# Performance work log

Hardware: AMD Instinct MI355X
Metric: run time of the kernel (lower is better)

Reference implementation:

```python
import jax, jax.numpy as jnp
import numpy as np

B, W, F = 16384, 64, 120
EPS = 1e-3  # keras BatchNormalization default epsilon


def _bn(x, g, b, m, v):
    return g * (x - m) * jax.lax.rsqrt(v + EPS) + b


def setup_inputs() -> dict:
    key = jax.random.key(0)
    ks = jax.random.split(key, 32)
    n = lambda i, s: jax.random.normal(ks[i], s, dtype=jnp.float32) * 0.05
    u = lambda i, s: jax.random.uniform(ks[i], s, dtype=jnp.float32) + 0.5
    W3 = W * 3
    return {
        'x': jax.random.normal(ks[0], (B, W, F), dtype=jnp.float32),
        # per-timestep Conv1D: only center tap matters on length-1 seq -> [W, F, 3]
        'conv_w': n(1, (W, F, 3)), 'conv_b': n(2, (W, 3)),
        # eye head
        'e_g1': u(3, (W3,)), 'e_b1': n(4, (W3,)), 'e_m1': n(5, (W3,)), 'e_v1': u(6, (W3,)),
        'e_d1_w': n(7, (W3, W3)), 'e_d1_b': n(8, (W3,)),
        'e_g2': u(9, (W3,)), 'e_b2': n(10, (W3,)), 'e_m2': n(11, (W3,)), 'e_v2': u(12, (W3,)),
        'e_d2_w': n(13, (W3, 2 * F)), 'e_d2_b': n(14, (2 * F,)),
        'e_d3_w': n(15, (2 * F, F)), 'e_d3_b': n(16, (F,)),
        # blink head
        'b_g1': u(17, (W3,)), 'b_b1': n(18, (W3,)), 'b_m1': n(19, (W3,)), 'b_v1': u(20, (W3,)),
        'b_d1_w': n(21, (W3, W)), 'b_d1_b': n(22, (W,)),
        'b_g2': u(23, (W,)), 'b_b2': n(24, (W,)), 'b_m2': n(25, (W,)), 'b_v2': u(26, (W,)),
        'b_d2_w': n(27, (W, W // 2)), 'b_d2_b': n(28, (W // 2,)),
        'b_d3_w': n(29, (W // 2, 1)), 'b_d3_b': n(30, (1,)),
    }


def reference(x, conv_w, conv_b, e_g1, e_b1, e_m1, e_v1, e_d1_w, e_d1_b,
              e_g2, e_b2, e_m2, e_v2, e_d2_w, e_d2_b, e_d3_w, e_d3_b,
              b_g1, b_b1, b_m1, b_v1, b_d1_w, b_d1_b,
              b_g2, b_b2, b_m2, b_v2, b_d2_w, b_d2_b, b_d3_w, b_d3_b):
    # window_size independent Conv1D(k=3,'same') on length-1 sequences reduce to a
    # single batched per-timestep matmul with the center kernel tap.
    combined = jnp.tanh(jnp.einsum('bwf,wfk->bwk', x, conv_w) + conv_b)
    combined = combined.reshape(x.shape[0], -1)  # [B, 3*W]
    # eye-feature head (dropout = identity at inference, BN uses moving stats)
    e = _bn(combined, e_g1, e_b1, e_m1, e_v1)
    e = jnp.tanh(e @ e_d1_w + e_d1_b)
    e = _bn(e, e_g2, e_b2, e_m2, e_v2)
    e = e @ e_d2_w + e_d2_b
    e = e @ e_d3_w + e_d3_b  # [B, F]
    # blink head
    b = _bn(combined, b_g1, b_b1, b_m1, b_v1)
    b = jnp.tanh(b @ b_d1_w + b_d1_b)
    b = _bn(b, b_g2, b_b2, b_m2, b_v2)
    b = jnp.tanh(b @ b_d2_w + b_d2_b)
    b = jax.nn.sigmoid(b @ b_d3_w + b_d3_b)  # [B, 1]
    return jnp.concatenate([e, b], axis=-1)  # [B, F+1]
```

## Files before the change

### kernel.cpp

```cpp
#include <hip/hip_runtime.h>
#include <hip/hip_bf16.h>
#include <string.h>

#define EPSBN 1e-3f

constexpr int kC1  = 192;
constexpr int kN2  = 240;
constexpr int kOut = 121;
constexpr int BTOT = 16384;

typedef __attribute__((ext_vector_type(8))) short bf16x8;
typedef __attribute__((ext_vector_type(4))) float f32x4;

__device__ __forceinline__ unsigned short f2bf(float f) {
  union { float f; unsigned u; } v; v.f = f;
  unsigned r = v.u + 0x7FFFu + ((v.u >> 16) & 1u);
  return (unsigned short)(r >> 16);
}
__device__ __forceinline__ float bf2f(unsigned short h) {
  union { unsigned u; float f; } v; v.u = ((unsigned)h) << 16;
  return v.f;
}

constexpr size_t OFF_W1E  = 0;
constexpr size_t OFF_W2E  = OFF_W1E + 73728;
constexpr size_t OFF_W3E  = OFF_W2E + 92160;
constexpr size_t OFF_W1B  = OFF_W3E + 65536;
constexpr size_t OFF_W2B  = OFF_W1B + 24576;
constexpr size_t OFF_BIAS = OFF_W2B + 4096;
constexpr size_t OFF_CWT  = OFF_BIAS + 2736;
constexpr size_t WS_NEED  = OFF_CWT + 122880;

__global__ __launch_bounds__(256) void prep_cwt(const float* __restrict__ cw,
                                                float* __restrict__ cwt4)
{
  int idx = blockIdx.x * 256 + threadIdx.x;
  if (idx < 7680) {
    int f = idx >> 6, w = idx & 63;
    float4 v;
    v.x = cw[(size_t)w * 360 + f * 3 + 0];
    v.y = cw[(size_t)w * 360 + f * 3 + 1];
    v.z = cw[(size_t)w * 360 + f * 3 + 2];
    v.w = 0.f;
    *reinterpret_cast<float4*>(cwt4 + (size_t)idx * 4) = v;
  }
}

__device__ __forceinline__ void pack_one(unsigned short* dst, int idx,
                                         const float* __restrict__ W, int Ksrc, int Nsrc,
                                         int KS, const float* g, const float* v)
{
  int per_nt = KS * 512;
  int nt = idx / per_nt; int r = idx - nt * per_nt;
  int ks = r >> 9; int r2 = r & 511;
  int l = r2 >> 3; int j = r2 & 7;
  int i = ks * 32 + ((l >> 4) << 3) + j;
  int n = (nt << 4) + (l & 15);
  float val = 0.f;
  if (i < Ksrc && n < Nsrc) {
    float s = g ? g[i] * rsqrtf(v[i] + EPSBN) : 1.f;
    val = s * W[(size_t)i * Nsrc + n];
  }
  dst[idx] = f2bf(val);
}

__global__ __launch_bounds__(256) void prep_pack(
    const float* e_g1, const float* e_v1, const float* e_d1_w,
    const float* e_g2, const float* e_v2, const float* e_d2_w,
    const float* e_d3_w,
    const float* b_g1, const float* b_v1, const float* b_d1_w,
    const float* b_g2, const float* b_v2, const float* b_d2_w,
    unsigned short* W1E, unsigned short* W2E, unsigned short* W3E,
    unsigned short* W1B, unsigned short* W2B)
{
  int e = blockIdx.x * 256 + threadIdx.x;
  if (e < 36864)                       pack_one(W1E, e,          e_d1_w, 192, 192, 6, e_g1, e_v1);
  else if (e < 36864 + 46080)          pack_one(W2E, e - 36864,  e_d2_w, 192, 240, 6, e_g2, e_v2);
  else if (e < 82944 + 32768)          pack_one(W3E, e - 82944,  e_d3_w, 240, 120, 8, nullptr, nullptr);
  else if (e < 115712 + 12288)         pack_one(W1B, e - 115712, b_d1_w, 192, 64,  6, b_g1, b_v1);
  else if (e < 128000 + 2048)          pack_one(W2B, e - 128000, b_d2_w, 64,  32,  2, b_g2, b_v2);
}

__global__ __launch_bounds__(256) void prep_bias(
    const float* e_g1, const float* e_b1, const float* e_m1, const float* e_v1,
    const float* e_d1_w, const float* e_d1_b,
    const float* e_g2, const float* e_b2, const float* e_m2, const float* e_v2,
    const float* e_d2_w, const float* e_d2_b, const float* e_d3_b,
    const float* b_g1, const float* b_b1, const float* b_m1, const float* b_v1,
    const float* b_d1_w, const float* b_d1_b,
    const float* b_g2, const float* b_b2, const float* b_m2, const float* b_v2,
    const float* b_d2_w, const float* b_d2_b,
    const float* b_d3_w, const float* b_d3_b,
    float* BIAS)
{
  int q = blockIdx.x * 256 + threadIdx.x;
  if (q < 192) {
    int j = q; float acc = e_d1_b[j];
    for (int i = 0; i < 192; ++i) {
      float s = e_g1[i] * rsqrtf(e_v1[i] + EPSBN);
      acc += (e_b1[i] - e_m1[i] * s) * e_d1_w[(size_t)i * 192 + j];
    }
    BIAS[q] = acc;
  } else if (q < 432) {
    int j = q - 192; float acc = e_d2_b[j];
    for (int i = 0; i < 192; ++i) {
      float s = e_g2[i] * rsqrtf(e_v2[i] + EPSBN);
      acc += (e_b2[i] - e_m2[i] * s) * e_d2_w[(size_t)i * 240 + j];
    }
    BIAS[q] = acc;
  } else if (q < 552) {
    BIAS[q] = e_d3_b[q - 432];
  } else if (q < 616) {
    int j = q - 552; float acc = b_d1_b[j];
    for (int i = 0; i < 192; ++i) {
      float s = b_g1[i] * rsqrtf(b_v1[i] + EPSBN);
      acc += (b_b1[i] - b_m1[i] * s) * b_d1_w[(size_t)i * 64 + j];
    }
    BIAS[q] = acc;
  } else if (q < 648) {
    int j = q - 616; float acc = b_d2_b[j];
    for (int i = 0; i < 64; ++i) {
      float s = b_g2[i] * rsqrtf(b_v2[i] + EPSBN);
      acc += (b_b2[i] - b_m2[i] * s) * b_d2_w[(size_t)i * 32 + j];
    }
    BIAS[q] = acc;
  } else if (q < 680) {
    BIAS[q] = b_d3_w[q - 648];
  } else if (q == 680) {
    BIAS[q] = b_d3_b[0];
  }
}

__global__ __launch_bounds__(64) void fused_all(
    const float* __restrict__ x,
    const float* __restrict__ cwt4, const float* __restrict__ conv_b,
    const unsigned short* __restrict__ W1E, const unsigned short* __restrict__ W2E,
    const unsigned short* __restrict__ W3E, const unsigned short* __restrict__ W1B,
    const unsigned short* __restrict__ W2B, const float* __restrict__ BIAS,
    float* __restrict__ out)
{
  __shared__ __align__(16) short Ac[16 * 200];
  __shared__ __align__(16) char  ubuf[15 * 65 * 16];

  float4* xt = reinterpret_cast<float4*>(ubuf);
  short*  Hs = reinterpret_cast<short*>(ubuf);
  short*  H2 = reinterpret_cast<short*>(ubuf + 6400);

  const int l = threadIdx.x;
  const int R = blockIdx.x * 16;

  {
    const float bc0 = conv_b[l * 3 + 0];
    const float bc1 = conv_b[l * 3 + 1];
    const float bc2 = conv_b[l * 3 + 2];

    for (int r = 0; r < 16; ++r) {
      const float* xrow = x + (size_t)(R + r) * 7680;
      float a0 = 0.f, a1 = 0.f, a2 = 0.f;

      for (int h = 0; h < 2; ++h) {
        #pragma unroll
        for (int i = 0; i < 15; ++i) {
          int g = i * 64 + l;
          int w = g / 15, fs = g - 15 * w;
          float4 v = *reinterpret_cast<const float4*>(xrow + w * 120 + h * 60 + 4 * fs);
          xt[fs * 65 + w] = v;
        }
        __syncthreads();

        #pragma unroll 5
        for (int fq = 0; fq < 15; ++fq) {
          float4 x4 = xt[fq * 65 + l];
          float xs[4] = {x4.x, x4.y, x4.z, x4.w};
          #pragma unroll
          for (int j = 0; j < 4; ++j) {
            int f = h * 60 + 4 * fq + j;
            float4 c4 = *reinterpret_cast<const float4*>(cwt4 + (size_t)(f * 64 + l) * 4);
            a0 = fmaf(xs[j], c4.x, a0);
            a1 = fmaf(xs[j], c4.y, a1);
            a2 = fmaf(xs[j], c4.z, a2);
          }
        }
        __syncthreads();
      }

      Ac[r * 200 + 3 * l + 0] = (short)f2bf(tanhf(a0 + bc0));
      Ac[r * 200 + 3 * l + 1] = (short)f2bf(tanhf(a1 + bc1));
      Ac[r * 200 + 3 * l + 2] = (short)f2bf(tanhf(a2 + bc2));
    }
  }
  __syncthreads();

  #pragma unroll
  for (int e = l; e < 256; e += 64) {
    int row = e >> 4, c = e & 15;
    H2[row * 264 + 240 + c] = 0;
  }

  const int arow = l & 15;
  const int kofs = (l >> 4) * 8;
  const int mb   = (l >> 4) * 4;

  for (int nt = 0; nt < 12; ++nt) {
    f32x4 acc = {0.f, 0.f, 0.f, 0.f};
    const bf16x8* bp = (const bf16x8*)W1E + (size_t)(nt * 6) * 64 + l;
    #pragma unroll
    for (int ks = 0; ks < 6; ++ks) {
      bf16x8 a = *(const bf16x8*)(Ac + arow * 200 + ks * 32 + kofs);
      acc = __builtin_amdgcn_mfma_f32_16x16x32_bf16(a, bp[(size_t)ks * 64], acc, 0, 0, 0);
    }
    int n = nt * 16 + arow;
    float bv = BIAS[n];
    __syncthreads();
    #pragma unroll
    for (int r = 0; r < 4; ++r)
      Hs[(mb + r) * 200 + n] = (short)f2bf(tanhf(acc[r] + bv));
  }
  __syncthreads();

  for (int nt = 0; nt < 15; ++nt) {
    f32x4 acc = {0.f, 0.f, 0.f, 0.f};
    const bf16x8* bp = (const bf16x8*)W2E + (size_t)(nt * 6) * 64 + l;
    #pragma unroll
    for (int ks = 0; ks < 6; ++ks) {
      bf16x8 a = *(const bf16x8*)(Hs + arow * 200 + ks * 32 + kofs);
      acc = __builtin_amdgcn_mfma_f32_16x16x32_bf16(a, bp[(size_t)ks * 64], acc, 0, 0, 0);
    }
    int n = nt * 16 + arow;
    float bv = BIAS[192 + n];
    #pragma unroll
    for (int r = 0; r < 4; ++r)
      H2[(mb + r) * 264 + n] = (short)f2bf(acc[r] + bv);
  }
  __syncthreads();

  for (int nt = 0; nt < 8; ++nt) {
    f32x4 acc = {0.f, 0.f, 0.f, 0.f};
    const bf16x8* bp = (const bf16x8*)W3E + (size_t)(nt * 8) * 64 + l;
    #pragma unroll
    for (int ks = 0; ks < 8; ++ks) {
      bf16x8 a = *(const bf16x8*)(H2 + arow * 264 + ks * 32 + kofs);
      acc = __builtin_amdgcn_mfma_f32_16x16x32_bf16(a, bp[(size_t)ks * 64], acc, 0, 0, 0);
    }
    int n = nt * 16 + arow;
    if (n < 120) {
      float bv = BIAS[432 + n];
      #pragma unroll
      for (int r = 0; r < 4; ++r)
        out[(size_t)(R + mb + r) * kOut + n] = acc[r] + bv;
    }
  }
  __syncthreads();

  for (int nt = 0; nt < 4; ++nt) {
    f32x4 acc = {0.f, 0.f, 0.f, 0.f};
    const bf16x8* bp = (const bf16x8*)W1B + (size_t)(nt * 6) * 64 + l;
    #pragma unroll
    for (int ks = 0; ks < 6; ++ks) {
      bf16x8 a = *(const bf16x8*)(Ac + arow * 200 + ks * 32 + kofs);
      acc = __builtin_amdgcn_mfma_f32_16x16x32_bf16(a, bp[(size_t)ks * 64], acc, 0, 0, 0);
    }
    int n = nt * 16 + arow;
    float bv = BIAS[552 + n];
    #pragma unroll
    for (int r = 0; r < 4; ++r)
      Hs[(mb + r) * 200 + n] = (short)f2bf(tanhf(acc[r] + bv));
  }
  __syncthreads();

  for (int nt = 0; nt < 2; ++nt) {
    f32x4 acc = {0.f, 0.f, 0.f, 0.f};
    const bf16x8* bp = (const bf16x8*)W2B + (size_t)(nt * 2) * 64 + l;
    #pragma unroll
    for (int ks = 0; ks < 2; ++ks) {
      bf16x8 a = *(const bf16x8*)(Hs + arow * 200 + ks * 32 + kofs);
      acc = __builtin_amdgcn_mfma_f32_16x16x32_bf16(a, bp[(size_t)ks * 64], acc, 0, 0, 0);
    }
    int n = nt * 16 + arow;
    float bv = BIAS[616 + n];
    #pragma unroll
    for (int r = 0; r < 4; ++r)
      H2[(mb + r) * 264 + n] = (short)f2bf(tanhf(acc[r] + bv));
  }
  __syncthreads();

  if (l < 16) {
    float s = BIAS[680];
    #pragma unroll
    for (int i = 0; i < 32; ++i)
      s = fmaf(bf2f((unsigned short)H2[l * 264 + i]), BIAS[648 + i], s);
    out[(size_t)(R + l) * kOut + 120] = 1.f / (1.f + expf(-s));
  }
}

constexpr int CSTR = 193;
__global__ __launch_bounds__(64, 4) void fused_blink_fb(
    const float* __restrict__ x,
    const float* __restrict__ conv_w, const float* __restrict__ conv_b,
    const float* __restrict__ e_g1, const float* __restrict__ e_b1,
    const float* __restrict__ e_m1, const float* __restrict__ e_v1,
    const float* __restrict__ e_d1_w, const float* __restrict__ e_d1_b,
    const float* __restrict__ e_g2, const float* __restrict__ e_b2,
    const float* __restrict__ e_m2, const float* __restrict__ e_v2,
    const float* __restrict__ e_d2_w, const float* __restrict__ e_d2_b,
    const float* __restrict__ e_d3_w, const float* __restrict__ e_d3_b,
    const float* __restrict__ b_g1, const float* __restrict__ b_b1,
    const float* __restrict__ b_m1, const float* __restrict__ b_v1,
    const float* __restrict__ b_d1_w, const float* __restrict__ b_d1_b,
    const float* __restrict__ b_g2, const float* __restrict__ b_b2,
    const float* __restrict__ b_m2, const float* __restrict__ b_v2,
    const float* __restrict__ b_d2_w, const float* __restrict__ b_d2_b,
    const float* __restrict__ b_d3_w, const float* __restrict__ b_d3_b,
    float* __restrict__ out)
{
  __shared__ float comb[4 * CSTR];
  __shared__ __align__(16) float Ab[4 * kN2];
  __shared__ __align__(16) float Bb[4 * kN2];
  const int lane = threadIdx.x;
  const int b0   = blockIdx.x * 4;
  {
    const int rcv = lane >> 4, wloc = lane & 15;
    for (int wc = 0; wc < 4; ++wc) {
      const int w = wc * 16 + wloc;
      const float* xr  = x + ((size_t)(b0 + rcv) * 64 + w) * 120;
      const float* cwp = conv_w + (size_t)w * 360;
      float a0 = 0.f, a1 = 0.f, a2 = 0.f;
      for (int t = 0; t < 30; ++t) {
        float4 xv = *reinterpret_cast<const float4*>(xr + 4 * t);
        float4 c0 = *reinterpret_cast<const float4*>(cwp + 12 * t);
        float4 c1 = *reinterpret_cast<const float4*>(cwp + 12 * t + 4);
        float4 c2 = *reinterpret_cast<const float4*>(cwp + 12 * t + 8);
        a0 += xv.x * c0.x + xv.y * c0.w + xv.z * c1.z + xv.w * c2.y;
        a1 += xv.x * c0.y + xv.y * c1.x + xv.z * c1.w + xv.w * c2.z;
        a2 += xv.x * c0.z + xv.y * c1.y + xv.z * c2.x + xv.w * c2.w;
      }
      comb[rcv * CSTR + 3 * w + 0] = tanhf(a0 + conv_b[3 * w + 0]);
      comb[rcv * CSTR + 3 * w + 1] = tanhf(a1 + conv_b[3 * w + 1]);
      comb[rcv * CSTR + 3 * w + 2] = tanhf(a2 + conv_b[3 * w + 2]);
    }
  }
  __syncthreads();
  #define AR(rr) (Ab + (size_t)(rr) * kN2)
  #define BR(rr) (Bb + (size_t)(rr) * kN2)
  #pragma unroll
  for (int q = 0; q < 12; ++q) {
    int rr = q / 3, cc = q % 3;
    int i = cc * 64 + lane;
    float s = e_g1[i] * rsqrtf(e_v1[i] + EPSBN);
    AR(rr)[i] = comb[rr * CSTR + i] * s + (e_b1[i] - e_m1[i] * s);
  }
  __syncthreads();
  {
    float acc[4][3];
    #pragma unroll
    for (int rr = 0; rr < 4; ++rr) { acc[rr][0]=acc[rr][1]=acc[rr][2]=0.f; }
    for (int i = 0; i < kC1; i += 4) {
      float4 v[4];
      #pragma unroll
      for (int rr = 0; rr < 4; ++rr) v[rr] = *reinterpret_cast<const float4*>(AR(rr) + i);
      #pragma unroll
      for (int io = 0; io < 4; ++io) {
        const float* wp = e_d1_w + (size_t)(i + io) * kC1 + lane;
        float w0 = wp[0], w1 = wp[64], w2 = wp[128];
        #pragma unroll
        for (int rr = 0; rr < 4; ++rr) {
          float xv = reinterpret_cast<const float*>(&v[rr])[io];
          acc[rr][0] = fmaf(xv, w0, acc[rr][0]);
          acc[rr][1] = fmaf(xv, w1, acc[rr][1]);
          acc[rr][2] = fmaf(xv, w2, acc[rr][2]);
        }
      }
    }
    #pragma unroll
    for (int c = 0; c < 3; ++c) {
      int j = c * 64 + lane;
      float s  = e_g2[j] * rsqrtf(e_v2[j] + EPSBN);
      float t  = e_b2[j] - e_m2[j] * s;
      float bs = e_d1_b[j];
      #pragma unroll
      for (int rr = 0; rr < 4; ++rr)
        BR(rr)[j] = tanhf(acc[rr][c] + bs) * s + t;
    }
  }
  __syncthreads();
  {
    const bool m3 = (lane < 48);
    float acc[4][4];
    #pragma unroll
    for (int rr = 0; rr < 4; ++rr) { acc[rr][0]=acc[rr][1]=acc[rr][2]=acc[rr][3]=0.f; }
    for (int i = 0; i < kC1; i += 4) {
      float4 v[4];
      #pragma unroll
      for (int rr = 0; rr < 4; ++rr) v[rr] = *reinterpret_cast<const float4*>(BR(rr) + i);
      #pragma unroll
      for (int io = 0; io < 4; ++io) {
        const float* wp = e_d2_w + (size_t)(i + io) * kN2 + lane;
        float w0 = wp[0], w1 = wp[64], w2 = wp[128];
        float w3 = m3 ? wp[192] : 0.f;
        #pragma unroll
        for (int rr = 0; rr < 4; ++rr) {
          float xv = reinterpret_cast<const float*>(&v[rr])[io];
          acc[rr][0] = fmaf(xv, w0, acc[rr][0]);
          acc[rr][1] = fmaf(xv, w1, acc[rr][1]);
          acc[rr][2] = fmaf(xv, w2, acc[rr][2]);
          acc[rr][3] = fmaf(xv, w3, acc[rr][3]);
        }
      }
    }
    #pragma unroll
    for (int c = 0; c < 4; ++c) {
      int j = c * 64 + lane;
      if (c < 3 || m3) {
        float bs = e_d2_b[j];
        #pragma unroll
        for (int rr = 0; rr < 4; ++rr)
          AR(rr)[j] = acc[rr][c] + bs;
      }
    }
  }
  __syncthreads();
  #pragma unroll
  for (int q = 0; q < 12; ++q) {
    int rr = q / 3, cc = q % 3;
    int i = cc * 64 + lane;
    float s = b_g1[i] * rsqrtf(b_v1[i] + EPSBN);
    BR(rr)[i] = comb[rr * CSTR + i] * s + (b_b1[i] - b_m1[i] * s);
  }
  {
    const bool m56 = (lane < 56);
    float acc[4][2];
    #pragma unroll
    for (int rr = 0; rr < 4; ++rr) { acc[rr][0]=acc[rr][1]=0.f; }
    for (int i = 0; i < kN2; i += 4) {
      float4 v[4];
      #pragma unroll
      for (int rr = 0; rr < 4; ++rr) v[rr] = *reinterpret_cast<const float4*>(AR(rr) + i);
      #pragma unroll
      for (int io = 0; io < 4; ++io) {
        const float* wp = e_d3_w + (size_t)(i + io) * 120 + lane;
        float w0 = wp[0];
        float w1 = m56 ? wp[64] : 0.f;
        #pragma unroll
        for (int rr = 0; rr < 4; ++rr) {
          float xv = reinterpret_cast<const float*>(&v[rr])[io];
          acc[rr][0] = fmaf(xv, w0, acc[rr][0]);
          acc[rr][1] = fmaf(xv, w1, acc[rr][1]);
        }
      }
    }
    #pragma unroll
    for (int c = 0; c < 2; ++c) {
      int j = c * 64 + lane;
      if (j < 120) {
        float bs = e_d3_b[j];
        #pragma unroll
        for (int rr = 0; rr < 4; ++rr)
          out[(size_t)(b0 + rr) * kOut + j] = acc[rr][c] + bs;
      }
    }
  }
  __syncthreads();
  {
    float acc[4] = {0.f, 0.f, 0.f, 0.f};
    for (int i = 0; i < kC1; i += 4) {
      float4 v[4];
      #pragma unroll
      for (int rr = 0; rr < 4; ++rr) v[rr] = *reinterpret_cast<const float4*>(BR(rr) + i);
      #pragma unroll
      for (int io = 0; io < 4; ++io) {
        float w0 = b_d1_w[(size_t)(i + io) * 64 + lane];
        #pragma unroll
        for (int rr = 0; rr < 4; ++rr) {
          float xv = reinterpret_cast<const float*>(&v[rr])[io];
          acc[rr] = fmaf(xv, w0, acc[rr]);
        }
      }
    }
    float s  = b_g2[lane] * rsqrtf(b_v2[lane] + EPSBN);
    float t  = b_b2[lane] - b_m2[lane] * s;
    float bs = b_d1_b[lane];
    #pragma unroll
    for (int rr = 0; rr < 4; ++rr)
      AR(rr)[lane] = tanhf(acc[rr] + bs) * s + t;
  }
  __syncthreads();
  {
    const bool m32 = (lane < 32);
    float acc[4] = {0.f, 0.f, 0.f, 0.f};
    for (int i = 0; i < 64; i += 4) {
      float4 v[4];
      #pragma unroll
      for (int rr = 0; rr < 4; ++rr) v[rr] = *reinterpret_cast<const float4*>(AR(rr) + i);
      #pragma unroll
      for (int io = 0; io < 4; ++io) {
        float w0 = m32 ? b_d2_w[(size_t)(i + io) * 32 + lane] : 0.f;
        #pragma unroll
        for (int rr = 0; rr < 4; ++rr) {
          float xv = reinterpret_cast<const float*>(&v[rr])[io];
          acc[rr] = fmaf(xv, w0, acc[rr]);
        }
      }
    }
    if (m32) {
      float bs = b_d2_b[lane];
      #pragma unroll
      for (int rr = 0; rr < 4; ++rr)
        BR(rr)[lane] = tanhf(acc[rr] + bs);
    }
  }
  __syncthreads();
  if (lane < 4) {
    int rr = lane;
    float acc = b_d3_b[0];
    #pragma unroll
    for (int i = 0; i < 32; ++i)
      acc = fmaf(BR(rr)[i], b_d3_w[i], acc);
    out[(size_t)(b0 + rr) * kOut + 120] = 1.f / (1.f + expf(-acc));
  }
  #undef AR
  #undef BR
}

extern "C" void kernel_launch(void* const* d_in, const int* in_sizes, int n_in,
                              void* d_out, int out_size, void* d_ws, size_t ws_size,
                              hipStream_t stream) {
  (void)in_sizes; (void)n_in; (void)out_size;
  const float* p[31];
  for (int i = 0; i < 31; ++i) p[i] = (const float*)d_in[i];
  float* out = (float*)d_out;

  if (ws_size >= WS_NEED && d_ws != nullptr) {
    char* ws = (char*)d_ws;
    unsigned short* W1E = (unsigned short*)(ws + OFF_W1E);
    unsigned short* W2E = (unsigned short*)(ws + OFF_W2E);
    unsigned short* W3E = (unsigned short*)(ws + OFF_W3E);
    unsigned short* W1B = (unsigned short*)(ws + OFF_W1B);
    unsigned short* W2B = (unsigned short*)(ws + OFF_W2B);
    float* BIAS         = (float*)(ws + OFF_BIAS);
    float* cwt4         = (float*)(ws + OFF_CWT);

    hipLaunchKernelGGL(prep_cwt, dim3(30), dim3(256), 0, stream, p[1], cwt4);
    hipLaunchKernelGGL(prep_pack, dim3(508), dim3(256), 0, stream,
                       p[3], p[6], p[7], p[9], p[12], p[13], p[15],
                       p[17], p[20], p[21], p[23], p[26], p[27],
                       W1E, W2E, W3E, W1B, W2B);
    hipLaunchKernelGGL(prep_bias, dim3(3), dim3(256), 0, stream,
                       p[3], p[4], p[5], p[6], p[7], p[8],
                       p[9], p[10], p[11], p[12], p[13], p[14], p[16],
                       p[17], p[18], p[19], p[20], p[21], p[22],
                       p[23], p[24], p[25], p[26], p[27], p[28],
                       p[29], p[30], BIAS);
    hipLaunchKernelGGL(fused_all, dim3(BTOT / 16), dim3(64), 0, stream,
                       p[0], cwt4, p[2], W1E, W2E, W3E, W1B, W2B, BIAS, out);
  } else {
    hipLaunchKernelGGL(fused_blink_fb, dim3(BTOT / 4), dim3(64), 0, stream,
      p[0], p[1], p[2], p[3], p[4], p[5], p[6], p[7], p[8], p[9],
      p[10], p[11], p[12], p[13], p[14], p[15], p[16], p[17], p[18], p[19],
      p[20], p[21], p[22], p[23], p[24], p[25], p[26], p[27], p[28], p[29], p[30],
      out);
  }
}
```

Baseline: 187.2 us.

## Stage conv weights in LDS per F-chunk and reuse across 16 rows

The per-timestep conv stage now loops over 10 chunks of 12 features and stages each chunk's conv weights in shared memory once. Those weights are then reused across all 16 rows of the block, with 48 per-row accumulators held in registers. The next row's x slice is prefetched into registers while the current row is computed. The aim is to stop re-reading the conv weights from global memory for every row, at the cost of higher register pressure and more barriers.

Result: slower. 328.0 us (+75.3%).

```diff
diff --git a/kernel.cpp b/kernel.cpp
--- a/kernel.cpp
+++ b/kernel.cpp
@@ -140,61 +140,84 @@
     float* __restrict__ out)
 {
   __shared__ __align__(16) short Ac[16 * 200];
-  __shared__ __align__(16) char  ubuf[15 * 65 * 16];
-
-  float4* xt = reinterpret_cast<float4*>(ubuf);
-  short*  Hs = reinterpret_cast<short*>(ubuf);
-  short*  H2 = reinterpret_cast<short*>(ubuf + 6400);
+  __shared__ __align__(16) char  ubuf[15424];
+
+  float4* cwt_s = reinterpret_cast<float4*>(ubuf);
+  float4* xt3   = reinterpret_cast<float4*>(ubuf + 12288);
+  short*  Hs    = reinterpret_cast<short*>(ubuf);
+  short*  H2    = reinterpret_cast<short*>(ubuf + 6400);
 
   const int l = threadIdx.x;
   const int R = blockIdx.x * 16;
 
   {
+    int wi[3], ji[3];
+    #pragma unroll
+    for (int i = 0; i < 3; ++i) { int g = i * 64 + l; wi[i] = g / 3; ji[i] = g - 3 * wi[i]; }
+
+    float acc[16][3];
+    #pragma unroll
+    for (int r = 0; r < 16; ++r) { acc[r][0] = acc[r][1] = acc[r][2] = 0.f; }
+
+    const float* xb = x + (size_t)R * 7680;
+
+    #pragma unroll 1
+    for (int c = 0; c < 10; ++c) {
+      const float4* cws = reinterpret_cast<const float4*>(cwt4) + (size_t)c * 768;
+      #pragma unroll
+      for (int i = 0; i < 12; ++i)
+        cwt_s[i * 64 + l] = cws[i * 64 + l];
+
+      float4 v[3];
+      #pragma unroll
+      for (int i = 0; i < 3; ++i)
+        v[i] = *reinterpret_cast<const float4*>(xb + (size_t)wi[i] * 120 + c * 12 + 4 * ji[i]);
+
+      __syncthreads();
+
+      #pragma unroll
+      for (int r = 0; r < 16; ++r) {
+        #pragma unroll
+        for (int i = 0; i < 3; ++i)
+          xt3[ji[i] * 65 + wi[i]] = v[i];
+        __syncthreads();
+        if (r < 15) {
+          #pragma unroll
+          for (int i = 0; i < 3; ++i)
+            v[i] = *reinterpret_cast<const float4*>(xb + (size_t)(r + 1) * 7680 + (size_t)wi[i] * 120 + c * 12 + 4 * ji[i]);
+        }
+        #pragma unroll
+        for (int j = 0; j < 3; ++j) {
+          float4 x4 = xt3[j * 65 + l];
+          float xs[4] = {x4.x, x4.y, x4.z, x4.w};
+          #pragma unroll
+          for (int jj = 0; jj < 4; ++jj) {
+            float4 c4 = cwt_s[(4 * j + jj) * 64 + l];
+            acc[r][0] = fmaf(xs[jj], c4.x, acc[r][0]);
+            acc[r][1] = fmaf(xs[jj], c4.y, acc[r][1]);
+            acc[r][2] = fmaf(xs[jj], c4.z, acc[r][2]);
+          }
+        }
+        __syncthreads();
+      }
+    }
+
     const float bc0 = conv_b[l * 3 + 0];
     const float bc1 = conv_b[l * 3 + 1];
     const float bc2 = conv_b[l * 3 + 2];
-
+    #pragma unroll
     for (int r = 0; r < 16; ++r) {
-      const float* xrow = x + (size_t)(R + r) * 7680;
-      float a0 = 0.f, a1 = 0.f, a2 = 0.f;
-
-      for (int h = 0; h < 2; ++h) {
-        #pragma unroll
-        for (int i = 0; i < 15; ++i) {
-          int g = i * 64 + l;
-          int w = g / 15, fs = g - 15 * w;
-          float4 v = *reinterpret_cast<const float4*>(xrow + w * 120 + h * 60 + 4 * fs);
-          xt[fs * 65 + w] = v;
-        }
-        __syncthreads();
-
-        #pragma unroll 5
-        for (int fq = 0; fq < 15; ++fq) {
-          float4 x4 = xt[fq * 65 + l];
-          float xs[4] = {x4.x, x4.y, x4.z, x4.w};
-          #pragma unroll
-          for (int j = 0; j < 4; ++j) {
-            int f = h * 60 + 4 * fq + j;
-            float4 c4 = *reinterpret_cast<const float4*>(cwt4 + (size_t)(f * 64 + l) * 4);
-            a0 = fmaf(xs[j], c4.x, a0);
-            a1 = fmaf(xs[j], c4.y, a1);
-            a2 = fmaf(xs[j], c4.z, a2);
-          }
-        }
-        __syncthreads();
-      }
-
-      Ac[r * 200 + 3 * l + 0] = (short)f2bf(tanhf(a0 + bc0));
-      Ac[r * 200 + 3 * l + 1] = (short)f2bf(tanhf(a1 + bc1));
-      Ac[r * 200 + 3 * l + 2] = (short)f2bf(tanhf(a2 + bc2));
+      Ac[r * 200 + 3 * l + 0] = (short)f2bf(tanhf(acc[r][0] + bc0));
+      Ac[r * 200 + 3 * l + 1] = (short)f2bf(tanhf(acc[r][1] + bc1));
+      Ac[r * 200 + 3 * l + 2] = (short)f2bf(tanhf(acc[r][2] + bc2));
     }
   }
   __syncthreads();
 
   #pragma unroll
   for (int e = l; e < 256; e += 64) {
-    int row = e >> 4, c = e & 15;
-    H2[row * 264 + 240 + c] = 0;
+    int row = e >> 4, cc = e & 15;
+    H2[row * 264 + 240 + cc] = 0;
   }
 
   const int arow = l & 15;
```

## Split fused kernel work across two waves per block

Applied to the files above, without the earlier changes.

Doubles the block to 128 threads. Each wave computes the conv projection for 8 of the block's 16 rows, using its own private LDS transpose buffer, and the MFMA dense layers split their output tiles between the two waves. One redundant barrier inside the first GEMM loop and one between the eye and blink heads are removed. The aim is more latency hiding and parallelism per block, at the cost of roughly doubled LDS per block, which may reduce resident blocks per CU.

Measured after the change: 197.8 us. 5.7% more time.

```diff
diff --git a/kernel.cpp b/kernel.cpp
--- a/kernel.cpp
+++ b/kernel.cpp
@@ -131,7 +131,7 @@
   }
 }
 
-__global__ __launch_bounds__(64) void fused_all(
+__global__ __launch_bounds__(128) void fused_all(
     const float* __restrict__ x,
     const float* __restrict__ cwt4, const float* __restrict__ conv_b,
     const unsigned short* __restrict__ W1E, const unsigned short* __restrict__ W2E,
@@ -140,22 +140,25 @@
     float* __restrict__ out)
 {
   __shared__ __align__(16) short Ac[16 * 200];
-  __shared__ __align__(16) char  ubuf[15 * 65 * 16];
-
-  float4* xt = reinterpret_cast<float4*>(ubuf);
-  short*  Hs = reinterpret_cast<short*>(ubuf);
-  short*  H2 = reinterpret_cast<short*>(ubuf + 6400);
-
-  const int l = threadIdx.x;
-  const int R = blockIdx.x * 16;
+  __shared__ __align__(16) char  ubuf[31200];
+
+  const int tid = threadIdx.x;
+  const int v   = tid >> 6;
+  const int l   = tid & 63;
+  const int R   = blockIdx.x * 16;
+
+  float4* xtv = reinterpret_cast<float4*>(ubuf + v * 15600);
+  short*  Hs  = reinterpret_cast<short*>(ubuf);
+  short*  H2  = reinterpret_cast<short*>(ubuf + 6400);
 
   {
     const float bc0 = conv_b[l * 3 + 0];
     const float bc1 = conv_b[l * 3 + 1];
     const float bc2 = conv_b[l * 3 + 2];
 
-    for (int r = 0; r < 16; ++r) {
-      const float* xrow = x + (size_t)(R + r) * 7680;
+    for (int r = 0; r < 8; ++r) {
+      const int row = 8 * v + r;
+      const float* xrow = x + (size_t)(R + row) * 7680;
       float a0 = 0.f, a1 = 0.f, a2 = 0.f;
 
       for (int h = 0; h < 2; ++h) {
@@ -163,14 +166,14 @@
         for (int i = 0; i < 15; ++i) {
           int g = i * 64 + l;
           int w = g / 15, fs = g - 15 * w;
-          float4 v = *reinterpret_cast<const float4*>(xrow + w * 120 + h * 60 + 4 * fs);
-          xt[fs * 65 + w] = v;
+          float4 vv = *reinterpret_cast<const float4*>(xrow + w * 120 + h * 60 + 4 * fs);
+          xtv[fs * 65 + w] = vv;
         }
         __syncthreads();
 
         #pragma unroll 5
         for (int fq = 0; fq < 15; ++fq) {
-          float4 x4 = xt[fq * 65 + l];
+          float4 x4 = xtv[fq * 65 + l];
           float xs[4] = {x4.x, x4.y, x4.z, x4.w};
           #pragma unroll
           for (int j = 0; j < 4; ++j) {
@@ -184,24 +187,24 @@
         __syncthreads();
       }
 
-      Ac[r * 200 + 3 * l + 0] = (short)f2bf(tanhf(a0 + bc0));
-      Ac[r * 200 + 3 * l + 1] = (short)f2bf(tanhf(a1 + bc1));
-      Ac[r * 200 + 3 * l + 2] = (short)f2bf(tanhf(a2 + bc2));
-    }
-  }
-  __syncthreads();
-
-  #pragma unroll
-  for (int e = l; e < 256; e += 64) {
-    int row = e >> 4, c = e & 15;
-    H2[row * 264 + 240 + c] = 0;
-  }
+      Ac[row * 200 + 3 * l + 0] = (short)f2bf(tanhf(a0 + bc0));
+      Ac[row * 200 + 3 * l + 1] = (short)f2bf(tanhf(a1 + bc1));
+      Ac[row * 200 + 3 * l + 2] = (short)f2bf(tanhf(a2 + bc2));
+    }
+  }
+  __syncthreads();
+
+  for (int e = tid; e < 256; e += 128) {
+    int row = e >> 4, cc = e & 15;
+    H2[row * 264 + 240 + cc] = 0;
+  }
+  __syncthreads();
 
   const int arow = l & 15;
   const int kofs = (l >> 4) * 8;
   const int mb   = (l >> 4) * 4;
 
-  for (int nt = 0; nt < 12; ++nt) {
+  for (int nt = 6 * v; nt < 6 * v + 6; ++nt) {
     f32x4 acc = {0.f, 0.f, 0.f, 0.f};
     const bf16x8* bp = (const bf16x8*)W1E + (size_t)(nt * 6) * 64 + l;
     #pragma unroll
@@ -211,14 +214,13 @@
     }
     int n = nt * 16 + arow;
     float bv = BIAS[n];
-    __syncthreads();
     #pragma unroll
     for (int r = 0; r < 4; ++r)
       Hs[(mb + r) * 200 + n] = (short)f2bf(tanhf(acc[r] + bv));
   }
   __syncthreads();
 
-  for (int nt = 0; nt < 15; ++nt) {
+  for (int nt = v ? 8 : 0; nt < (v ? 15 : 8); ++nt) {
     f32x4 acc = {0.f, 0.f, 0.f, 0.f};
     const bf16x8* bp = (const bf16x8*)W2E + (size_t)(nt * 6) * 64 + l;
     #pragma unroll
@@ -234,7 +236,7 @@
   }
   __syncthreads();
 
-  for (int nt = 0; nt < 8; ++nt) {
+  for (int nt = 4 * v; nt < 4 * v + 4; ++nt) {
     f32x4 acc = {0.f, 0.f, 0.f, 0.f};
     const bf16x8* bp = (const bf16x8*)W3E + (size_t)(nt * 8) * 64 + l;
     #pragma unroll
@@ -250,9 +252,7 @@
         out[(size_t)(R + mb + r) * kOut + n] = acc[r] + bv;
     }
   }
-  __syncthreads();
-
-  for (int nt = 0; nt < 4; ++nt) {
+  for (int nt = 2 * v; nt < 2 * v + 2; ++nt) {
     f32x4 acc = {0.f, 0.f, 0.f, 0.f};
     const bf16x8* bp = (const bf16x8*)W1B + (size_t)(nt * 6) * 64 + l;
     #pragma unroll
@@ -268,7 +268,8 @@
   }
   __syncthreads();
 
-  for (int nt = 0; nt < 2; ++nt) {
+  {
+    int nt = v;
     f32x4 acc = {0.f, 0.f, 0.f, 0.f};
     const bf16x8* bp = (const bf16x8*)W2B + (size_t)(nt * 2) * 64 + l;
     #pragma unroll
@@ -284,7 +285,7 @@
   }
   __syncthreads();
 
-  if (l < 16) {
+  if (v == 0 && l < 16) {
     float s = BIAS[680];
     #pragma unroll
     for (int i = 0; i < 32; ++i)
@@ -550,7 +551,7 @@
                        p[17], p[18], p[19], p[20], p[21], p[22],
                        p[23], p[24], p[25], p[26], p[27], p[28],
                        p[29], p[30], BIAS);
-    hipLaunchKernelGGL(fused_all, dim3(BTOT / 16), dim3(64), 0, stream,
+    hipLaunchKernelGGL(fused_all, dim3(BTOT / 16), dim3(128), 0, stream,
                        p[0], cwt4, p[2], W1E, W2E, W3E, W1B, W2B, BIAS, out);
   } else {
     hipLaunchKernelGGL(fused_blink_fb, dim3(BTOT / 4), dim3(64), 0, stream,
```
